# Performance work log

Hardware: AMD Instinct MI355X
Metric: run time of the kernel (lower is better)

## Reference

```python
import jax, jax.numpy as jnp
import numpy as np

B, N, NPOINT, NSAMPLE = 8, 16384, 512, 64
RADIUS = 0.1
C_IN = 64
DIMS = [64, 64, 128]


def setup_inputs() -> dict:
    key = jax.random.key(0)
    ks = jax.random.split(key, 8)
    xyz = jax.random.uniform(ks[0], (B, N, 3), jnp.float32)          # points in unit cube
    features = jax.random.normal(ks[1], (B, C_IN, N), jnp.float32)   # (B, C, N) per GroupGatherByIndex
    dims = [3 + C_IN] + DIMS                                         # use_xyz_feature adds 3
    out = {"xyz": xyz, "features": features}
    for i in range(3):
        out[f"W{i+1}"] = jax.random.normal(ks[2 + i], (dims[i], dims[i + 1]), jnp.float32) / np.sqrt(dims[i])
        out[f"b{i+1}"] = jnp.zeros((dims[i + 1],), jnp.float32)
    return out


def furthest_point_sampling(xyz, npoint):
    # Iterative FPS starting at index 0 (matches CUDA kernel semantics).
    Bq, Nq, _ = xyz.shape
    barange = jnp.arange(Bq)

    def step(carry, _):
        dists, last = carry
        p = xyz[barange, last]                       # (B, 3)
        d = jnp.sum((xyz - p[:, None, :]) ** 2, -1)  # (B, N)
        dists = jnp.minimum(dists, d)
        nxt = jnp.argmax(dists, axis=1).astype(jnp.int32)
        return (dists, nxt), nxt

    init = (jnp.full((Bq, Nq), 1e10, xyz.dtype), jnp.zeros((Bq,), jnp.int32))
    _, idxs = jax.lax.scan(step, init, None, length=npoint - 1)
    return jnp.concatenate([jnp.zeros((Bq, 1), jnp.int32), idxs.T], axis=1)  # (B, npoint)


def ball_query(new_xyz, xyz, radius, nsample):
    # For each centroid, first nsample in-ball indices (ascending), padded with first hit.
    Nq = xyz.shape[1]
    d2 = jnp.sum((new_xyz[:, :, None, :] - xyz[:, None, :, :]) ** 2, -1)  # (B, npoint, N)
    cand = jnp.where(d2 < radius * radius, jnp.arange(Nq, dtype=jnp.int32), Nq)
    cand = jnp.sort(cand, axis=-1)[..., :nsample]                          # (B, npoint, nsample)
    first = jnp.where(cand[..., :1] == Nq, 0, cand[..., :1])
    return jnp.where(cand == Nq, first, cand)


def reference(xyz, features, W1, b1, W2, b2, W3, b3):
    fps_idx = furthest_point_sampling(xyz, NPOINT)                  # (B, npoint)
    new_xyz = jax.vmap(lambda p, i: p[i])(xyz, fps_idx)             # (B, npoint, 3)
    idx = ball_query(new_xyz, xyz, RADIUS, NSAMPLE)                 # (B, npoint, nsample)
    grouped_xyz = jax.vmap(lambda p, i: p[i])(xyz, idx)             # (B, npoint, nsample, 3)
    centered = grouped_xyz - new_xyz[:, :, None, :]                 # centroid subtract
    feats_n = jnp.transpose(features, (0, 2, 1))                    # (B, N, C)
    grouped_f = jax.vmap(lambda f, i: f[i])(feats_n, idx)           # (B, npoint, nsample, C)
    h = jnp.concatenate([centered, grouped_f], axis=-1)             # (B, npoint, nsample, 3+C)
    for W, b in ((W1, b1), (W2, b2), (W3, b3)):                     # pointwise 1x1-conv MLP + ReLU
        h = jax.nn.relu(h @ W + b)
    return jnp.max(h, axis=2)                                       # max-pool over nsample -> (B, npoint, C_out)
```

## Files before the change

kernel.cpp:

```cpp
#include <hip/hip_runtime.h>

#define NB 8
#define NPTS 16384
#define NPOINT 512
#define NSAMPLE 64
#define CIN 64
#define PPT 16

typedef float v2f __attribute__((ext_vector_type(2)));

template <int CTRL>
__device__ __forceinline__ float dpp_f(float x) {
    int xi = __builtin_bit_cast(int, x);
    int yi = __builtin_amdgcn_update_dpp(xi, xi, CTRL, 0xF, 0xF, false);
    return __builtin_bit_cast(float, yi);
}
template <int CTRL>
__device__ __forceinline__ int dpp_i(int x) {
    return __builtin_amdgcn_update_dpp(x, x, CTRL, 0xF, 0xF, false);
}

__device__ __forceinline__ float wave_max_f(float x) {
    x = fmaxf(x, dpp_f<0x111>(x));
    x = fmaxf(x, dpp_f<0x112>(x));
    x = fmaxf(x, dpp_f<0x114>(x));
    x = fmaxf(x, dpp_f<0x118>(x));
    x = fmaxf(x, dpp_f<0x142>(x));
    x = fmaxf(x, dpp_f<0x143>(x));
    return x;
}
__device__ __forceinline__ int wave_min_i(int x) {
    x = min(x, dpp_i<0x111>(x));
    x = min(x, dpp_i<0x112>(x));
    x = min(x, dpp_i<0x114>(x));
    x = min(x, dpp_i<0x118>(x));
    x = min(x, dpp_i<0x142>(x));
    x = min(x, dpp_i<0x143>(x));
    return x;
}

__global__ __launch_bounds__(1024) __attribute__((amdgpu_waves_per_eu(4)))
void fps_transpose_kernel(
    const float* __restrict__ xyz, const float* __restrict__ feats,
    int* __restrict__ fps_idx, float* __restrict__ feats_t)
{
    __shared__ float t[64][65];
    __shared__ __align__(16) int s_pair[2][16][2];

    if (blockIdx.x >= NB) {
        int blk = blockIdx.x - NB;
        int b = blk & 7;
        int tile = blk >> 3;
        int n0 = tile * 64;
        int cc = threadIdx.x & 63, rr = threadIdx.x >> 6;
        const float* fb = feats + (size_t)b * CIN * NPTS;
        #pragma unroll
        for (int k = 0; k < 4; ++k) {
            int c = rr + k * 16;
            t[c][cc] = fb[(size_t)c * NPTS + n0 + cc];
        }
        __syncthreads();
        float* fo = feats_t + ((size_t)b * NPTS + n0) * CIN;
        #pragma unroll
        for (int k = 0; k < 4; ++k) {
            int n = rr + k * 16;
            fo[n * CIN + cc] = t[cc][n];
        }
        return;
    }

    const int b = blockIdx.x;
    const int tid = threadIdx.x;
    const int wv = tid >> 6, ln = tid & 63;
    const float* xb = xyz + (size_t)b * NPTS * 3;
    const int base = tid * PPT;

    v2f px2[8], py2[8], pz2[8], dd2[8];
    {
        const float4* xb4 = (const float4*)(xb + (size_t)base * 3);
        #pragma unroll
        for (int q = 0; q < 4; ++q) {
            float4 f0 = xb4[3 * q + 0];
            float4 f1 = xb4[3 * q + 1];
            float4 f2 = xb4[3 * q + 2];
            px2[2 * q + 0] = (v2f){f0.x, f0.w};
            py2[2 * q + 0] = (v2f){f0.y, f1.x};
            pz2[2 * q + 0] = (v2f){f0.z, f1.y};
            px2[2 * q + 1] = (v2f){f1.z, f2.y};
            py2[2 * q + 1] = (v2f){f1.w, f2.z};
            pz2[2 * q + 1] = (v2f){f2.x, f2.w};
        }
        #pragma unroll
        for (int k = 0; k < 8; ++k) dd2[k] = (v2f){1e10f, 1e10f};
    }
    if (tid == 0) fps_idx[b * NPOINT] = 0;
    float cx = xb[0], cy = xb[1], cz = xb[2];
    __syncthreads();

    for (int j = 1; j < NPOINT; ++j) {
        #pragma clang fp contract(off)
        const int p = j & 1;
        v2f ncx = (v2f){-cx, -cx};
        v2f ncy = (v2f){-cy, -cy};
        v2f ncz = (v2f){-cz, -cz};
        float bm = -1.0f;
        #pragma unroll
        for (int k = 0; k < 8; ++k) {
            v2f dx = px2[k] + ncx;
            v2f dy = py2[k] + ncy;
            v2f dz = pz2[k] + ncz;
            v2f s1 = dx * dx + dy * dy;
            v2f d2 = s1 + dz * dz;
            v2f nd = __builtin_elementwise_min(dd2[k], d2);
            dd2[k] = nd;
            bm = fmaxf(bm, fmaxf(nd.x, nd.y));
        }
        float wm = wave_max_f(bm);
        float wmax = __builtin_bit_cast(float,
            __builtin_amdgcn_readlane(__builtin_bit_cast(int, wm), 63));
        int mk = 64;
        #pragma unroll
        for (int k = 0; k < 8; ++k) {
            int ca = (dd2[k].x == wmax) ? (2 * k)     : 64;
            int cb = (dd2[k].y == wmax) ? (2 * k + 1) : 64;
            mk = min(mk, min(ca, cb));
        }
        int mi = (mk == 64) ? 0x7fffffff : (base + mk);
        int rm = wave_min_i(mi);
        int wave_mi = __builtin_amdgcn_readlane(rm, 63);
        if (ln == 0) {
            s_pair[p][wv][0] = __builtin_bit_cast(int, wmax);
            s_pair[p][wv][1] = wave_mi;
        }
        __syncthreads();
        int2 pr = *(const int2*)&s_pair[p][ln & 15][0];
        float v = __builtin_bit_cast(float, pr.x);
        int   i = pr.y;
        {
            float ov; int oi; bool tk;
            ov = dpp_f<0x111>(v); oi = dpp_i<0x111>(i);
            tk = (ov > v) || (ov == v && oi < i); v = tk ? ov : v; i = tk ? oi : i;
            ov = dpp_f<0x112>(v); oi = dpp_i<0x112>(i);
            tk = (ov > v) || (ov == v && oi < i); v = tk ? ov : v; i = tk ? oi : i;
            ov = dpp_f<0x114>(v); oi = dpp_i<0x114>(i);
            tk = (ov > v) || (ov == v && oi < i); v = tk ? ov : v; i = tk ? oi : i;
            ov = dpp_f<0x118>(v); oi = dpp_i<0x118>(i);
            tk = (ov > v) || (ov == v && oi < i); v = tk ? ov : v; i = tk ? oi : i;
        }
        int ch = __builtin_amdgcn_readlane(i, 15);
        const float* cp = xb + 3 * ch;
        cx = cp[0]; cy = cp[1]; cz = cp[2];
        if (tid == 0) fps_idx[b * NPOINT + j] = ch;
    }
}

__global__ __launch_bounds__(64) void ballmlp_kernel(
    const float* __restrict__ xyz, const float* __restrict__ feats_t,
    const int* __restrict__ fps_idx,
    const float* __restrict__ W1, const float* __restrict__ b1,
    const float* __restrict__ W2, const float* __restrict__ b2,
    const float* __restrict__ W3, const float* __restrict__ b3,
    float* __restrict__ out)
{
    const float R2 = (float)(0.1 * 0.1);
    int blk = blockIdx.x;
    int b = blk & 7, j = blk >> 3;
    int s = threadIdx.x;
    int cent = b * NPOINT + j;
    const float* xb = xyz + (size_t)b * NPTS * 3;

    __shared__ float X[67][64];
    __shared__ int slots[64];

    int cidx = fps_idx[cent];
    float cx = xb[3 * cidx + 0];
    float cy = xb[3 * cidx + 1];
    float cz = xb[3 * cidx + 2];

    int cnt = 0;
    for (int bs = 0; bs < NPTS; bs += 64) {
        int i = bs + s;
        float dx = __fsub_rn(xb[3 * i + 0], cx);
        float dy = __fsub_rn(xb[3 * i + 1], cy);
        float dz = __fsub_rn(xb[3 * i + 2], cz);
        float d2 = __fadd_rn(__fadd_rn(__fmul_rn(dx, dx), __fmul_rn(dy, dy)), __fmul_rn(dz, dz));
        bool inb = d2 < R2;
        unsigned long long m = __ballot(inb);
        int pre = (int)__popcll(m & ((1ull << s) - 1ull));
        int slot = cnt + pre;
        if (inb && slot < NSAMPLE) slots[slot] = i;
        cnt += (int)__popcll(m);
        if (cnt >= NSAMPLE) break;
    }
    __syncthreads();
    int first = (cnt > 0) ? slots[0] : 0;
    int i = (s < cnt) ? slots[s] : first;

    const float* pp = xyz + ((size_t)b * NPTS + i) * 3;
    X[64][s] = pp[0] - cx;
    X[65][s] = pp[1] - cy;
    X[66][s] = pp[2] - cz;
    const float4* fr = (const float4*)(feats_t + ((size_t)b * NPTS + i) * CIN);
    #pragma unroll
    for (int q = 0; q < 16; ++q) {
        float4 f = fr[q];
        X[q * 4 + 0][s] = f.x;
        X[q * 4 + 1][s] = f.y;
        X[q * 4 + 2][s] = f.z;
        X[q * 4 + 3][s] = f.w;
    }

    float acc[64];
    #pragma unroll
    for (int o = 0; o < 64; ++o) acc[o] = b1[o];
    for (int c = 0; c < 67; ++c) {
        float xc = X[c][s];
        const float* w = W1 + ((c < 64) ? (c + 3) : (c - 64)) * 64;
        #pragma unroll
        for (int o = 0; o < 64; ++o) acc[o] = fmaf(xc, w[o], acc[o]);
    }
    #pragma unroll
    for (int o = 0; o < 64; ++o) X[o][s] = fmaxf(acc[o], 0.0f);

    #pragma unroll
    for (int o = 0; o < 64; ++o) acc[o] = b2[o];
    for (int c = 0; c < 64; ++c) {
        float xc = X[c][s];
        const float* w = W2 + c * 64;
        #pragma unroll
        for (int o = 0; o < 64; ++o) acc[o] = fmaf(xc, w[o], acc[o]);
    }
    #pragma unroll
    for (int o = 0; o < 64; ++o) X[o][s] = fmaxf(acc[o], 0.0f);

    float h3[128];
    #pragma unroll
    for (int o = 0; o < 128; ++o) h3[o] = b3[o];
    for (int c = 0; c < 64; ++c) {
        float xc = X[c][s];
        const float* w = W3 + c * 128;
        #pragma unroll
        for (int o = 0; o < 128; ++o) h3[o] = fmaf(xc, w[o], h3[o]);
    }

    #pragma unroll
    for (int o = 0; o < 128; ++o)
        h3[o] = wave_max_f(fmaxf(h3[o], 0.0f));
    if (s == 63) {
        float* op = out + (size_t)cent * 128;
        #pragma unroll
        for (int o = 0; o < 128; o += 4) {
            float4 v = make_float4(h3[o], h3[o + 1], h3[o + 2], h3[o + 3]);
            *(float4*)&op[o] = v;
        }
    }
}

extern "C" void kernel_launch(void* const* d_in, const int* in_sizes, int n_in,
                              void* d_out, int out_size, void* d_ws, size_t ws_size,
                              hipStream_t stream) {
    const float* xyz   = (const float*)d_in[0];
    const float* feats = (const float*)d_in[1];
    const float* W1 = (const float*)d_in[2];
    const float* b1 = (const float*)d_in[3];
    const float* W2 = (const float*)d_in[4];
    const float* b2 = (const float*)d_in[5];
    const float* W3 = (const float*)d_in[6];
    const float* b3 = (const float*)d_in[7];
    float* out = (float*)d_out;

    char* ws = (char*)d_ws;
    int*   fps_idx  = (int*)ws;
    float* feats_t  = (float*)(ws + 65536);

    fps_transpose_kernel<<<NB + NB * (NPTS / 64), 1024, 0, stream>>>(xyz, feats, fps_idx, feats_t);
    ballmlp_kernel<<<NB * NPOINT, 64, 0, stream>>>(xyz, feats_t, fps_idx,
                                                   W1, b1, W2, b2, W3, b3, out);
}
```

Before: 1.241 ms.

## Split FPS into SoA prep plus 512-thread FPS with LDS-staged coordinates

Adds a prep kernel that transposes features and converts xyz into separate x/y/z arrays. FPS now runs as its own kernel with 512 threads per batch, each owning 32 points. Its x and y coordinates sit in LDS and z stays in registers. The winning wave publishes the chosen point's coordinates, so the global reload of the next centroid is gone, and the argmax index scan only runs in lanes holding the max. Ball query reads the SoA arrays for coalesced loads. The cost is an extra kernel launch, LDS reads every iteration, and FPS no longer overlapping with the transpose.

```diff
diff --git a/kernel.cpp b/kernel.cpp
--- a/kernel.cpp
+++ b/kernel.cpp
@@ -5,7 +5,6 @@
 #define NPOINT 512
 #define NSAMPLE 64
 #define CIN 64
-#define PPT 16
 
 typedef float v2f __attribute__((ext_vector_type(2)));
 
@@ -39,62 +38,81 @@
     return x;
 }
 
-__global__ __launch_bounds__(1024) __attribute__((amdgpu_waves_per_eu(4)))
-void fps_transpose_kernel(
-    const float* __restrict__ xyz, const float* __restrict__ feats,
-    int* __restrict__ fps_idx, float* __restrict__ feats_t)
+__global__ __launch_bounds__(256) void prep_kernel(
+    const float* __restrict__ feats, const float* __restrict__ xyz,
+    float* __restrict__ feats_t,
+    float* __restrict__ xs, float* __restrict__ ys, float* __restrict__ zs)
 {
+    int blk = blockIdx.x;
+    int tid = threadIdx.x;
+    if (blk >= 2048) {
+        int b = blk - 2048;
+        const float* xb = xyz + (size_t)b * NPTS * 3;
+        float* xsb = xs + (size_t)b * NPTS;
+        float* ysb = ys + (size_t)b * NPTS;
+        float* zsb = zs + (size_t)b * NPTS;
+        for (int k = 0; k < NPTS / 256; ++k) {
+            int i = k * 256 + tid;
+            xsb[i] = xb[3 * i + 0];
+            ysb[i] = xb[3 * i + 1];
+            zsb[i] = xb[3 * i + 2];
+        }
+        return;
+    }
     __shared__ float t[64][65];
-    __shared__ __align__(16) int s_pair[2][16][2];
-
-    if (blockIdx.x >= NB) {
-        int blk = blockIdx.x - NB;
-        int b = blk & 7;
-        int tile = blk >> 3;
-        int n0 = tile * 64;
-        int cc = threadIdx.x & 63, rr = threadIdx.x >> 6;
-        const float* fb = feats + (size_t)b * CIN * NPTS;
-        #pragma unroll
-        for (int k = 0; k < 4; ++k) {
-            int c = rr + k * 16;
-            t[c][cc] = fb[(size_t)c * NPTS + n0 + cc];
-        }
-        __syncthreads();
-        float* fo = feats_t + ((size_t)b * NPTS + n0) * CIN;
-        #pragma unroll
-        for (int k = 0; k < 4; ++k) {
-            int n = rr + k * 16;
-            fo[n * CIN + cc] = t[cc][n];
-        }
-        return;
-    }
+    int b = blk & 7, tile = blk >> 3, n0 = tile * 64;
+    int cc = tid & 63, rr = tid >> 6;
+    const float* fb = feats + (size_t)b * CIN * NPTS;
+    #pragma unroll
+    for (int k = 0; k < 16; ++k) {
+        int c = k * 4 + rr;
+        t[c][cc] = fb[(size_t)c * NPTS + n0 + cc];
+    }
+    __syncthreads();
+    float* fo = feats_t + ((size_t)b * NPTS + n0) * CIN;
+    #pragma unroll
+    for (int k = 0; k < 16; ++k) {
+        int n = k * 4 + rr;
+        fo[(size_t)n * CIN + cc] = t[cc][n];
+    }
+}
+
+__global__ __launch_bounds__(512) __attribute__((amdgpu_waves_per_eu(2, 2)))
+void fps_kernel(
+    const float* __restrict__ xs, const float* __restrict__ ys,
+    const float* __restrict__ zs, int* __restrict__ fps_idx)
+{
+    __shared__ float x_lds[8][512][4];
+    __shared__ float y_lds[8][512][4];
+    __shared__ __align__(16) int s_pub[2][8][8];
 
     const int b = blockIdx.x;
     const int tid = threadIdx.x;
     const int wv = tid >> 6, ln = tid & 63;
-    const float* xb = xyz + (size_t)b * NPTS * 3;
-    const int base = tid * PPT;
-
-    v2f px2[8], py2[8], pz2[8], dd2[8];
+    const float* xsb = xs + (size_t)b * NPTS;
+    const float* ysb = ys + (size_t)b * NPTS;
+    const float* zsb = zs + (size_t)b * NPTS;
+
+    v2f z2[16], dd2[16];
     {
-        const float4* xb4 = (const float4*)(xb + (size_t)base * 3);
-        #pragma unroll
-        for (int q = 0; q < 4; ++q) {
-            float4 f0 = xb4[3 * q + 0];
-            float4 f1 = xb4[3 * q + 1];
-            float4 f2 = xb4[3 * q + 2];
-            px2[2 * q + 0] = (v2f){f0.x, f0.w};
-            py2[2 * q + 0] = (v2f){f0.y, f1.x};
-            pz2[2 * q + 0] = (v2f){f0.z, f1.y};
-            px2[2 * q + 1] = (v2f){f1.z, f2.y};
-            py2[2 * q + 1] = (v2f){f1.w, f2.z};
-            pz2[2 * q + 1] = (v2f){f2.x, f2.w};
-        }
-        #pragma unroll
-        for (int k = 0; k < 8; ++k) dd2[k] = (v2f){1e10f, 1e10f};
+        const float4* XS4 = (const float4*)xsb;
+        const float4* YS4 = (const float4*)ysb;
+        const float4* ZS4 = (const float4*)zsb;
+        #pragma unroll
+        for (int g = 0; g < 8; ++g) {
+            float4 fx = XS4[tid * 8 + g];
+            float4 fy = YS4[tid * 8 + g];
+            float4 fz = ZS4[tid * 8 + g];
+            *(float4*)&x_lds[g][tid][0] = fx;
+            *(float4*)&y_lds[g][tid][0] = fy;
+            z2[2 * g + 0] = (v2f){fz.x, fz.y};
+            z2[2 * g + 1] = (v2f){fz.z, fz.w};
+        }
+        #pragma unroll
+        for (int m = 0; m < 16; ++m) dd2[m] = (v2f){1e10f, 1e10f};
     }
     if (tid == 0) fps_idx[b * NPOINT] = 0;
-    float cx = xb[0], cy = xb[1], cz = xb[2];
+    float cx = xsb[0], cy = ysb[0], cz = zsb[0];
     __syncthreads();
 
     for (int j = 1; j < NPOINT; ++j) {
@@ -105,58 +123,80 @@
         v2f ncz = (v2f){-cz, -cz};
         float bm = -1.0f;
         #pragma unroll
-        for (int k = 0; k < 8; ++k) {
-            v2f dx = px2[k] + ncx;
-            v2f dy = py2[k] + ncy;
-            v2f dz = pz2[k] + ncz;
-            v2f s1 = dx * dx + dy * dy;
-            v2f d2 = s1 + dz * dz;
-            v2f nd = __builtin_elementwise_min(dd2[k], d2);
-            dd2[k] = nd;
-            bm = fmaxf(bm, fmaxf(nd.x, nd.y));
+        for (int g = 0; g < 8; ++g) {
+            float4 fx = *(const float4*)&x_lds[g][tid][0];
+            float4 fy = *(const float4*)&y_lds[g][tid][0];
+            v2f dxl = (v2f){fx.x, fx.y} + ncx;
+            v2f dyl = (v2f){fy.x, fy.y} + ncy;
+            v2f dzl = z2[2 * g + 0] + ncz;
+            v2f d2l = (dxl * dxl + dyl * dyl) + dzl * dzl;
+            v2f ndl = __builtin_elementwise_min(dd2[2 * g + 0], d2l);
+            dd2[2 * g + 0] = ndl;
+            v2f dxh = (v2f){fx.z, fx.w} + ncx;
+            v2f dyh = (v2f){fy.z, fy.w} + ncy;
+            v2f dzh = z2[2 * g + 1] + ncz;
+            v2f d2h = (dxh * dxh + dyh * dyh) + dzh * dzh;
+            v2f ndh = __builtin_elementwise_min(dd2[2 * g + 1], d2h);
+            dd2[2 * g + 1] = ndh;
+            bm = fmaxf(bm, fmaxf(fmaxf(ndl.x, ndl.y), fmaxf(ndh.x, ndh.y)));
         }
         float wm = wave_max_f(bm);
         float wmax = __builtin_bit_cast(float,
             __builtin_amdgcn_readlane(__builtin_bit_cast(int, wm), 63));
-        int mk = 64;
-        #pragma unroll
-        for (int k = 0; k < 8; ++k) {
-            int ca = (dd2[k].x == wmax) ? (2 * k)     : 64;
-            int cb = (dd2[k].y == wmax) ? (2 * k + 1) : 64;
-            mk = min(mk, min(ca, cb));
-        }
-        int mi = (mk == 64) ? 0x7fffffff : (base + mk);
+        int mk = 32;
+        if (bm == wmax) {
+            #pragma unroll
+            for (int m = 15; m >= 0; --m) {
+                mk = (dd2[m].y == wmax) ? (2 * m + 1) : mk;
+                mk = (dd2[m].x == wmax) ? (2 * m)     : mk;
+            }
+        }
+        int mi = (mk == 32) ? 0x7fffffff : (tid * 32 + mk);
         int rm = wave_min_i(mi);
-        int wave_mi = __builtin_amdgcn_readlane(rm, 63);
-        if (ln == 0) {
-            s_pair[p][wv][0] = __builtin_bit_cast(int, wmax);
-            s_pair[p][wv][1] = wave_mi;
+        int wmi = __builtin_amdgcn_readlane(rm, 63);
+        if (mi == wmi && mk != 32) {
+            int g = mk >> 2, e = mk & 3;
+            float cpx = x_lds[g][tid][e];
+            float cpy = y_lds[g][tid][e];
+            float cpz = zsb[mi];
+            s_pub[p][wv][0] = __builtin_bit_cast(int, wmax);
+            s_pub[p][wv][1] = mi;
+            s_pub[p][wv][2] = __builtin_bit_cast(int, cpx);
+            s_pub[p][wv][3] = __builtin_bit_cast(int, cpy);
+            s_pub[p][wv][4] = __builtin_bit_cast(int, cpz);
         }
         __syncthreads();
-        int2 pr = *(const int2*)&s_pair[p][ln & 15][0];
-        float v = __builtin_bit_cast(float, pr.x);
-        int   i = pr.y;
+        int4 q = *(const int4*)&s_pub[p][ln & 7][0];
+        int qz = s_pub[p][ln & 7][4];
+        float v = __builtin_bit_cast(float, q.x);
+        int ii = q.y, xc = q.z, yc = q.w, zc = qz;
         {
-            float ov; int oi; bool tk;
-            ov = dpp_f<0x111>(v); oi = dpp_i<0x111>(i);
-            tk = (ov > v) || (ov == v && oi < i); v = tk ? ov : v; i = tk ? oi : i;
-            ov = dpp_f<0x112>(v); oi = dpp_i<0x112>(i);
-            tk = (ov > v) || (ov == v && oi < i); v = tk ? ov : v; i = tk ? oi : i;
-            ov = dpp_f<0x114>(v); oi = dpp_i<0x114>(i);
-            tk = (ov > v) || (ov == v && oi < i); v = tk ? ov : v; i = tk ? oi : i;
-            ov = dpp_f<0x118>(v); oi = dpp_i<0x118>(i);
-            tk = (ov > v) || (ov == v && oi < i); v = tk ? ov : v; i = tk ? oi : i;
-        }
-        int ch = __builtin_amdgcn_readlane(i, 15);
-        const float* cp = xb + 3 * ch;
-        cx = cp[0]; cy = cp[1]; cz = cp[2];
+            float ov; int oi, ox, oy, oz; bool tk;
+            ov = dpp_f<0x111>(v); oi = dpp_i<0x111>(ii);
+            ox = dpp_i<0x111>(xc); oy = dpp_i<0x111>(yc); oz = dpp_i<0x111>(zc);
+            tk = (ov > v) || (ov == v && oi < ii);
+            v = tk ? ov : v; ii = tk ? oi : ii; xc = tk ? ox : xc; yc = tk ? oy : yc; zc = tk ? oz : zc;
+            ov = dpp_f<0x112>(v); oi = dpp_i<0x112>(ii);
+            ox = dpp_i<0x112>(xc); oy = dpp_i<0x112>(yc); oz = dpp_i<0x112>(zc);
+            tk = (ov > v) || (ov == v && oi < ii);
+            v = tk ? ov : v; ii = tk ? oi : ii; xc = tk ? ox : xc; yc = tk ? oy : yc; zc = tk ? oz : zc;
+            ov = dpp_f<0x114>(v); oi = dpp_i<0x114>(ii);
+            ox = dpp_i<0x114>(xc); oy = dpp_i<0x114>(yc); oz = dpp_i<0x114>(zc);
+            tk = (ov > v) || (ov == v && oi < ii);
+            v = tk ? ov : v; ii = tk ? oi : ii; xc = tk ? ox : xc; yc = tk ? oy : yc; zc = tk ? oz : zc;
+        }
+        int ch = __builtin_amdgcn_readlane(ii, 7);
+        cx = __builtin_bit_cast(float, __builtin_amdgcn_readlane(xc, 7));
+        cy = __builtin_bit_cast(float, __builtin_amdgcn_readlane(yc, 7));
+        cz = __builtin_bit_cast(float, __builtin_amdgcn_readlane(zc, 7));
         if (tid == 0) fps_idx[b * NPOINT + j] = ch;
     }
 }
 
 __global__ __launch_bounds__(64) void ballmlp_kernel(
-    const float* __restrict__ xyz, const float* __restrict__ feats_t,
-    const int* __restrict__ fps_idx,
+    const float* __restrict__ xyz,
+    const float* __restrict__ xs, const float* __restrict__ ys, const float* __restrict__ zs,
+    const float* __restrict__ feats_t, const int* __restrict__ fps_idx,
     const float* __restrict__ W1, const float* __restrict__ b1,
     const float* __restrict__ W2, const float* __restrict__ b2,
     const float* __restrict__ W3, const float* __restrict__ b3,
@@ -167,22 +207,24 @@
     int b = blk & 7, j = blk >> 3;
     int s = threadIdx.x;
     int cent = b * NPOINT + j;
-    const float* xb = xyz + (size_t)b * NPTS * 3;
+    const float* xsb = xs + (size_t)b * NPTS;
+    const float* ysb = ys + (size_t)b * NPTS;
+    const float* zsb = zs + (size_t)b * NPTS;
 
     __shared__ float X[67][64];
     __shared__ int slots[64];
 
     int cidx = fps_idx[cent];
-    float cx = xb[3 * cidx + 0];
-    float cy = xb[3 * cidx + 1];
-    float cz = xb[3 * cidx + 2];
+    float cx = xsb[cidx];
+    float cy = ysb[cidx];
+    float cz = zsb[cidx];
 
     int cnt = 0;
     for (int bs = 0; bs < NPTS; bs += 64) {
         int i = bs + s;
-        float dx = __fsub_rn(xb[3 * i + 0], cx);
-        float dy = __fsub_rn(xb[3 * i + 1], cy);
-        float dz = __fsub_rn(xb[3 * i + 2], cz);
+        float dx = __fsub_rn(xsb[i], cx);
+        float dy = __fsub_rn(ysb[i], cy);
+        float dz = __fsub_rn(zsb[i], cz);
         float d2 = __fadd_rn(__fadd_rn(__fmul_rn(dx, dx), __fmul_rn(dy, dy)), __fmul_rn(dz, dz));
         bool inb = d2 < R2;
         unsigned long long m = __ballot(inb);
@@ -270,10 +312,14 @@
     float* out = (float*)d_out;
 
     char* ws = (char*)d_ws;
-    int*   fps_idx  = (int*)ws;
-    float* feats_t  = (float*)(ws + 65536);
-
-    fps_transpose_kernel<<<NB + NB * (NPTS / 64), 1024, 0, stream>>>(xyz, feats, fps_idx, feats_t);
-    ballmlp_kernel<<<NB * NPOINT, 64, 0, stream>>>(xyz, feats_t, fps_idx,
+    int*   fps_idx = (int*)ws;
+    float* xs = (float*)(ws + 16384);
+    float* ys = (float*)(ws + 16384 + 524288);
+    float* zs = (float*)(ws + 16384 + 2 * 524288);
+    float* feats_t = (float*)(ws + 16384 + 4 * 524288);
+
+    prep_kernel<<<2048 + NB, 256, 0, stream>>>(feats, xyz, feats_t, xs, ys, zs);
+    fps_kernel<<<NB, 512, 0, stream>>>(xs, ys, zs, fps_idx);
+    ballmlp_kernel<<<NB * NPOINT, 64, 0, stream>>>(xyz, xs, ys, zs, feats_t, fps_idx,
                                                    W1, b1, W2, b2, W3, b3, out);
 }
```

Result: slower. 1.295 ms (+4.4%).
